# Kernel optimization log

Hardware: AMD Instinct MI355X
Metric: run time of the kernel (lower is better)

Reference implementation:

```python
import jax, jax.numpy as jnp
import numpy as np

NUM_HEADS = 12


def setup_inputs() -> dict:
    key = jax.random.key(0)
    k1, k2, k3, k4 = jax.random.split(key, 4)
    B, N, C = 8, 1024, 768
    x = jax.random.normal(k1, (B, N, C), dtype=jnp.float32)
    w_qkv = jax.random.normal(k2, (3 * C, C), dtype=jnp.float32) * 0.02
    w_proj = jax.random.normal(k3, (C, C), dtype=jnp.float32) * 0.02
    b_proj = jax.random.normal(k4, (C,), dtype=jnp.float32) * 0.02
    return {"x": x, "w_qkv": w_qkv, "w_proj": w_proj, "b_proj": b_proj}


def reference(x, w_qkv, w_proj, b_proj):
    B, N, C = x.shape
    H = NUM_HEADS
    D = C // H
    scale = D ** -0.5
    # qkv projection (HMQLinear with quant=False is a plain linear, bias=False)
    qkv = jnp.einsum('bnc,oc->bno', x, w_qkv)          # [B,N,3C]
    qkv = qkv.reshape(B, N, 3, H, D).transpose(2, 0, 3, 1, 4)  # [3,B,H,N,D]
    q, k, v = qkv[0], qkv[1], qkv[2]
    # HMQMulQK (passthrough matmul), scale applied after QK^T as in source
    attn = jnp.einsum('bhqd,bhkd->bhqk', q, k) * scale  # [B,H,N,N]
    attn = jax.nn.softmax(attn, axis=-1)                # HMQSoftmax
    out = jnp.einsum('bhqk,bhkd->bhqd', attn, v)        # HMQMulSV
    out = out.transpose(0, 2, 1, 3).reshape(B, N, C)
    # output projection (HMQLinear, default bias=True)
    return jnp.einsum('bnc,oc->bno', out, w_proj) + b_proj
```

## Files before the change

kernel.cpp:

```cpp
#include <hip/hip_runtime.h>
#include <hip/hip_bf16.h>
#include <stdint.h>

typedef __attribute__((ext_vector_type(8))) short short8;
typedef __attribute__((ext_vector_type(4))) float f32x4;
typedef __attribute__((ext_vector_type(16))) float f32x16;
typedef __attribute__((ext_vector_type(4))) unsigned short us4;

__device__ inline unsigned short f2bf(float f) {
    unsigned int u = __float_as_uint(f);
    u += 0x7FFFu + ((u >> 16) & 1u);
    return (unsigned short)(u >> 16);
}

__device__ inline unsigned int cvtpk(float lo, float hi) {
    unsigned int r;
    asm("v_cvt_pk_bf16_f32 %0, %1, %2" : "=v"(r) : "v"(lo), "v"(hi));
    return r;
}

__device__ inline void pl32swap(unsigned int& a, unsigned int& b) {
    asm volatile("v_permlane32_swap_b32 %0, %1" : "+v"(a), "+v"(b));
}

__global__ void cvt_f32_bf16(const float* __restrict__ in,
                             unsigned short* __restrict__ out, int n4) {
    int i = blockIdx.x * blockDim.x + threadIdx.x;
    if (i >= n4) return;
    float4 v = ((const float4*)in)[i];
    us4 o;
    o.x = f2bf(v.x); o.y = f2bf(v.y); o.z = f2bf(v.z); o.w = f2bf(v.w);
    ((us4*)out)[i] = o;
}

#define BM 128
#define BN 128
#define BKK 32

template<int MODE>
__global__ __launch_bounds__(256)
void gemm_bt(const unsigned short* __restrict__ A,
             const unsigned short* __restrict__ Bm,
             unsigned short* __restrict__ Qo, unsigned short* __restrict__ Ko,
             unsigned short* __restrict__ Vto,
             float* __restrict__ Co, const float* __restrict__ bias,
             int M, int N, int K)
{
    __shared__ __align__(16) unsigned short As[2][BM * BKK];
    __shared__ __align__(16) unsigned short Bs[2][BN * BKK];
    const int tid = threadIdx.x;
    const int wave = tid >> 6, lane = tid & 63;
    const int tr = blockIdx.x * BM;
    const int tc = blockIdx.y * BN;
    const int wm = wave >> 1, wn = wave & 1;

    f32x4 acc[4][4] = {};

    const int srow = lane >> 2;
    const int scol = (lane & 3) * 8;

    auto stage = [&](int it, int buf) {
#pragma unroll
        for (int i = 0; i < 2; ++i) {
            int rb = (wave * 2 + i) * 16;
            __builtin_amdgcn_global_load_lds(
                (const __attribute__((address_space(1))) void*)(A + (size_t)(tr + rb + srow) * K + it * BKK + scol),
                (__attribute__((address_space(3))) void*)(&As[buf][rb * BKK]),
                16, 0, 0);
            __builtin_amdgcn_global_load_lds(
                (const __attribute__((address_space(1))) void*)(Bm + (size_t)(tc + rb + srow) * K + it * BKK + scol),
                (__attribute__((address_space(3))) void*)(&Bs[buf][rb * BKK]),
                16, 0, 0);
        }
    };

    const int nIt = K / BKK;
    stage(0, 0);
    __syncthreads();

    for (int it = 0; it < nIt; ++it) {
        const int cur = it & 1;
        if (it + 1 < nIt) stage(it + 1, cur ^ 1);

        short8 af[4], bf[4];
#pragma unroll
        for (int mt = 0; mt < 4; ++mt)
            af[mt] = *(const short8*)&As[cur][(wm * 64 + mt * 16 + (lane & 15)) * BKK + (lane >> 4) * 8];
#pragma unroll
        for (int nt = 0; nt < 4; ++nt)
            bf[nt] = *(const short8*)&Bs[cur][(wn * 64 + nt * 16 + (lane & 15)) * BKK + (lane >> 4) * 8];
#pragma unroll
        for (int mt = 0; mt < 4; ++mt)
#pragma unroll
            for (int nt = 0; nt < 4; ++nt)
                acc[mt][nt] = __builtin_amdgcn_mfma_f32_16x16x32_bf16(af[mt], bf[nt], acc[mt][nt], 0, 0, 0);
        __syncthreads();
    }

    const float QSCALE = 0.18033688011112042f;
#pragma unroll
    for (int mt = 0; mt < 4; ++mt) {
#pragma unroll
        for (int nt = 0; nt < 4; ++nt) {
            int col = tc + wn * 64 + nt * 16 + (lane & 15);
            int row0 = tr + wm * 64 + mt * 16 + (lane >> 4) * 4;
            if constexpr (MODE == 0) {
                int s = (col >= 1536) ? 2 : (col >= 768 ? 1 : 0);
                int rem = col - s * 768;
                int h = rem >> 6, d = rem & 63;
                int b = row0 >> 10, n0 = row0 & 1023;
                int bh = b * 12 + h;
                if (s == 2) {
                    us4 pv;
#pragma unroll
                    for (int r = 0; r < 4; ++r) pv[r] = f2bf(acc[mt][nt][r]);
                    *(us4*)&Vto[((size_t)bh * 64 + d) * 1024 + n0] = pv;
                } else {
                    unsigned short* dst = (s == 0) ? Qo : Ko;
                    float sc = (s == 0) ? QSCALE : 1.0f;
#pragma unroll
                    for (int r = 0; r < 4; ++r)
                        dst[((size_t)bh * 1024 + n0 + r) * 64 + d] = f2bf(acc[mt][nt][r] * sc);
                }
            } else {
#pragma unroll
                for (int r = 0; r < 4; ++r)
                    Co[(size_t)(row0 + r) * N + col] = acc[mt][nt][r] + bias[col];
            }
        }
    }
}

__global__ __launch_bounds__(256)
void attn_kernel(const unsigned short* __restrict__ Q,
                 const unsigned short* __restrict__ Kg,
                 const unsigned short* __restrict__ Vt,
                 unsigned short* __restrict__ Og)
{
    __shared__ __align__(16) unsigned short KV[2][2][64 * 64];

    const int tid = threadIdx.x;
    const int wave = tid >> 6, lane = tid & 63;
    const int l31 = lane & 31, hi = lane >> 5;
    const int bh = blockIdx.y;
    const int b = bh / 12, h = bh % 12;
    const size_t baseK = (size_t)bh * 1024 * 64;
    const size_t baseV = (size_t)bh * 64 * 1024;
    const int q0 = blockIdx.x * 128 + wave * 32;

    short8 qf[4];
#pragma unroll
    for (int ds = 0; ds < 4; ++ds)
        qf[ds] = *(const short8*)&Q[baseK + (size_t)(q0 + l31) * 64 + ds * 16 + hi * 8];

    f32x16 ot0 = {}, ot1 = {};
    float l = 0.f;

    auto stage = [&](int kt, int buf) {
        const unsigned short* gK = Kg + baseK + (size_t)kt * 64 * 64;
        const unsigned short* gV = Vt + baseV + kt * 64;
#pragma unroll
        for (int i = 0; i < 2; ++i) {
            int c = wave * 128 + i * 64 + lane;
            int r = c >> 3, cc = c & 7;
            int sw = (cc ^ (r & 7)) * 8;
            __builtin_amdgcn_global_load_lds(
                (const __attribute__((address_space(1))) void*)(gK + r * 64 + sw),
                (__attribute__((address_space(3))) void*)(&KV[buf][0][(wave * 128 + i * 64) * 8]),
                16, 0, 0);
            __builtin_amdgcn_global_load_lds(
                (const __attribute__((address_space(1))) void*)(gV + (size_t)r * 1024 + sw),
                (__attribute__((address_space(3))) void*)(&KV[buf][1][(wave * 128 + i * 64) * 8]),
                16, 0, 0);
        }
    };

    auto rfrag = [&](const unsigned short* s, int row, int cc) -> short8 {
        return *(const short8*)&s[(row * 8 + (cc ^ (row & 7))) * 8];
    };

    stage(0, 0);
    __syncthreads();

    for (int kt = 0; kt < 16; ++kt) {
        const int cur = kt & 1;
        if (kt < 15) stage(kt + 1, cur ^ 1);

        f32x16 st0 = {}, st1 = {};
        __builtin_amdgcn_s_setprio(1);
#pragma unroll
        for (int ds = 0; ds < 4; ++ds) {
            short8 k0 = rfrag(KV[cur][0], l31, ds * 2 + hi);
            short8 k1 = rfrag(KV[cur][0], 32 + l31, ds * 2 + hi);
            st0 = __builtin_amdgcn_mfma_f32_32x32x16_bf16(k0, qf[ds], st0, 0, 0, 0);
            st1 = __builtin_amdgcn_mfma_f32_32x32x16_bf16(k1, qf[ds], st1, 0, 0, 0);
        }
        __builtin_amdgcn_s_setprio(0);

#pragma unroll
        for (int i = 0; i < 16; ++i) {
            st0[i] = exp2f(st0[i]);
            st1[i] = exp2f(st1[i]);
        }
        float su[8];
#pragma unroll
        for (int i = 0; i < 8; ++i)
            su[i] = (st0[2 * i] + st0[2 * i + 1]) + (st1[2 * i] + st1[2 * i + 1]);
#pragma unroll
        for (int s = 4; s > 0; s >>= 1)
#pragma unroll
            for (int i = 0; i < 4; ++i)
                if (i < s) su[i] += su[i + s];
        float ps = su[0];
        {
            unsigned int pu = __float_as_uint(ps), pv = pu;
            pl32swap(pu, pv);
            float other = __uint_as_float(hi ? pv : pu);
            l += ps + other;
        }

        short8 paf[4];
#pragma unroll
        for (int kb = 0; kb < 4; ++kb) {
            unsigned int a0, a1, b0, b1;
            if (kb < 2) {
                int t0 = 8 * kb;
                a0 = cvtpk(st0[t0 + 0], st0[t0 + 1]);
                a1 = cvtpk(st0[t0 + 2], st0[t0 + 3]);
                b0 = cvtpk(st0[t0 + 4], st0[t0 + 5]);
                b1 = cvtpk(st0[t0 + 6], st0[t0 + 7]);
            } else {
                int t0 = 8 * (kb - 2);
                a0 = cvtpk(st1[t0 + 0], st1[t0 + 1]);
                a1 = cvtpk(st1[t0 + 2], st1[t0 + 3]);
                b0 = cvtpk(st1[t0 + 4], st1[t0 + 5]);
                b1 = cvtpk(st1[t0 + 6], st1[t0 + 7]);
            }
            pl32swap(a0, b0);
            pl32swap(a1, b1);
            union { unsigned int u[4]; short8 s; } fr;
            fr.u[0] = a0; fr.u[1] = a1; fr.u[2] = b0; fr.u[3] = b1;
            paf[kb] = fr.s;
        }

        __builtin_amdgcn_s_setprio(1);
#pragma unroll
        for (int kb = 0; kb < 4; ++kb) {
            short8 v0 = rfrag(KV[cur][1], l31, kb * 2 + hi);
            short8 v1 = rfrag(KV[cur][1], 32 + l31, kb * 2 + hi);
            ot0 = __builtin_amdgcn_mfma_f32_32x32x16_bf16(v0, paf[kb], ot0, 0, 0, 0);
            ot1 = __builtin_amdgcn_mfma_f32_32x32x16_bf16(v1, paf[kb], ot1, 0, 0, 0);
        }
        __builtin_amdgcn_s_setprio(0);

        __syncthreads();
    }

    float inv = 1.f / l;
#pragma unroll
    for (int i = 0; i < 16; ++i) { ot0[i] *= inv; ot1[i] *= inv; }

    unsigned int* ow = (unsigned int*)(&KV[0][0][0]) + wave * 1152;
#pragma unroll
    for (int dt = 0; dt < 2; ++dt)
#pragma unroll
        for (int rp = 0; rp < 8; ++rp) {
            unsigned int w = (dt == 0) ? cvtpk(ot0[2 * rp], ot0[2 * rp + 1])
                                       : cvtpk(ot1[2 * rp], ot1[2 * rp + 1]);
            int wd = dt * 16 + 4 * (rp >> 1) + 2 * hi + (rp & 1);
            ow[l31 * 36 + wd] = w;
        }
#pragma unroll
    for (int i = 0; i < 4; ++i) {
        int c = i * 64 + lane;
        int qr = c >> 3, ch = c & 7;
        short8 vv = *(const short8*)((const unsigned short*)&ow[qr * 36 + ch * 4]);
        *(short8*)&Og[(size_t)(b * 1024 + q0 + qr) * 768 + h * 64 + ch * 8] = vv;
    }
}

extern "C" void kernel_launch(void* const* d_in, const int* in_sizes, int n_in,
                              void* d_out, int out_size, void* d_ws, size_t ws_size,
                              hipStream_t stream) {
    const float* x      = (const float*)d_in[0];
    const float* w_qkv  = (const float*)d_in[1];
    const float* w_proj = (const float*)d_in[2];
    const float* b_proj = (const float*)d_in[3];
    float* out = (float*)d_out;

    const int Bb = 8, Nn = 1024, C = 768;
    const int M = Bb * Nn;
    const size_t XB = (size_t)M * C;
    const size_t WQ = (size_t)3 * C * C;
    const size_t WP = (size_t)C * C;
    const size_t QE = (size_t)96 * 1024 * 64;

    unsigned short* xb  = (unsigned short*)d_ws;
    unsigned short* wqb = xb + XB;
    unsigned short* wpb = wqb + WQ;
    unsigned short* Qb  = wpb + WP;
    unsigned short* Kb  = Qb + QE;
    unsigned short* Vtb = Kb + QE;
    unsigned short* AO  = Vtb + QE;

    cvt_f32_bf16<<<(int)(XB / 4 + 255) / 256, 256, 0, stream>>>(x, xb, (int)(XB / 4));
    cvt_f32_bf16<<<(int)(WQ / 4 + 255) / 256, 256, 0, stream>>>(w_qkv, wqb, (int)(WQ / 4));
    cvt_f32_bf16<<<(int)(WP / 4 + 255) / 256, 256, 0, stream>>>(w_proj, wpb, (int)(WP / 4));

    gemm_bt<0><<<dim3(M / BM, (3 * C) / BN), 256, 0, stream>>>(
        xb, wqb, Qb, Kb, Vtb, nullptr, nullptr, M, 3 * C, C);

    attn_kernel<<<dim3(Nn / 128, Bb * 12), 256, 0, stream>>>(Qb, Kb, Vtb, AO);

    gemm_bt<1><<<dim3(M / BM, C / BN), 256, 0, stream>>>(
        AO, wpb, nullptr, nullptr, nullptr, out, b_proj, M, C, C);
}
```

Before: 136.8 us.

## Permute V layout to drop permlane swaps, interleave softmax with PV MFMAs, fuse conversions

The V^T store in the QKV GEMM now permutes token positions within 16-element groups. This lets the attention kernel feed exp'd score registers straight into the PV MFMA without the permlane32 swaps. The attention loop is split so exp and pack of the first score tile overlap with PV MFMAs, and the row-sum cross-half reduction moves out of the loop. It also uses the native exp2 builtin, sets launch bounds for 3 blocks per CU, and merges the three f32-to-bf16 conversion launches into one. The risk is correctness: the layout permutation must exactly match the MFMA fragment mapping.

```diff
diff --git a/kernel.cpp b/kernel.cpp
--- a/kernel.cpp
+++ b/kernel.cpp
@@ -23,14 +23,29 @@
     asm volatile("v_permlane32_swap_b32 %0, %1" : "+v"(a), "+v"(b));
 }
 
-__global__ void cvt_f32_bf16(const float* __restrict__ in,
-                             unsigned short* __restrict__ out, int n4) {
+__device__ inline float fexp2(float x) {
+#if __has_builtin(__builtin_amdgcn_exp2f)
+    return __builtin_amdgcn_exp2f(x);
+#else
+    return exp2f(x);
+#endif
+}
+
+__global__ void cvt_all(const float* __restrict__ x, const float* __restrict__ wq,
+                        const float* __restrict__ wp,
+                        unsigned short* __restrict__ xb,
+                        unsigned short* __restrict__ wqb,
+                        unsigned short* __restrict__ wpb) {
+    const int X4 = 1572864, Q4 = 442368;
     int i = blockIdx.x * blockDim.x + threadIdx.x;
-    if (i >= n4) return;
-    float4 v = ((const float4*)in)[i];
+    const float* src; unsigned short* dst; int j;
+    if (i < X4) { src = x; dst = xb; j = i; }
+    else if (i < X4 + Q4) { src = wq; dst = wqb; j = i - X4; }
+    else { src = wp; dst = wpb; j = i - X4 - Q4; }
+    float4 v = ((const float4*)src)[j];
     us4 o;
     o.x = f2bf(v.x); o.y = f2bf(v.y); o.z = f2bf(v.z); o.w = f2bf(v.w);
-    ((us4*)out)[i] = o;
+    ((us4*)dst)[j] = o;
 }
 
 #define BM 128
@@ -114,7 +129,9 @@
                     us4 pv;
 #pragma unroll
                     for (int r = 0; r < 4; ++r) pv[r] = f2bf(acc[mt][nt][r]);
-                    *(us4*)&Vto[((size_t)bh * 64 + d) * 1024 + n0] = pv;
+                    int qd = (n0 >> 2) & 3;
+                    int nst = n0 + ((qd == 1) ? 4 : (qd == 2) ? -4 : 0);
+                    *(us4*)&Vto[((size_t)bh * 64 + d) * 1024 + nst] = pv;
                 } else {
                     unsigned short* dst = (s == 0) ? Qo : Ko;
                     float sc = (s == 0) ? QSCALE : 1.0f;
@@ -131,7 +148,7 @@
     }
 }
 
-__global__ __launch_bounds__(256)
+__global__ __launch_bounds__(256, 3)
 void attn_kernel(const unsigned short* __restrict__ Q,
                  const unsigned short* __restrict__ Kg,
                  const unsigned short* __restrict__ Vt,
@@ -179,6 +196,14 @@
         return *(const short8*)&s[(row * 8 + (cc ^ (row & 7))) * 8];
     };
 
+    auto pack8 = [&](const f32x16& S, int r0) -> short8 {
+        union { unsigned int u[4]; short8 s; } fr;
+#pragma unroll
+        for (int w = 0; w < 4; ++w)
+            fr.u[w] = cvtpk(S[r0 + 2 * w], S[r0 + 2 * w + 1]);
+        return fr.s;
+    };
+
     stage(0, 0);
     __syncthreads();
 
@@ -197,11 +222,39 @@
         }
         __builtin_amdgcn_s_setprio(0);
 
-#pragma unroll
-        for (int i = 0; i < 16; ++i) {
-            st0[i] = exp2f(st0[i]);
-            st1[i] = exp2f(st1[i]);
-        }
+        short8 v00 = rfrag(KV[cur][1], l31, 0 + hi);
+        short8 v10 = rfrag(KV[cur][1], 32 + l31, 0 + hi);
+        short8 v01 = rfrag(KV[cur][1], l31, 2 + hi);
+        short8 v11 = rfrag(KV[cur][1], 32 + l31, 2 + hi);
+
+#pragma unroll
+        for (int i = 0; i < 16; ++i) st0[i] = fexp2(st0[i]);
+        short8 paf0 = pack8(st0, 0);
+        short8 paf1 = pack8(st0, 8);
+
+        __builtin_amdgcn_s_setprio(1);
+        ot0 = __builtin_amdgcn_mfma_f32_32x32x16_bf16(v00, paf0, ot0, 0, 0, 0);
+        ot1 = __builtin_amdgcn_mfma_f32_32x32x16_bf16(v10, paf0, ot1, 0, 0, 0);
+        ot0 = __builtin_amdgcn_mfma_f32_32x32x16_bf16(v01, paf1, ot0, 0, 0, 0);
+        ot1 = __builtin_amdgcn_mfma_f32_32x32x16_bf16(v11, paf1, ot1, 0, 0, 0);
+        __builtin_amdgcn_s_setprio(0);
+
+        short8 v02 = rfrag(KV[cur][1], l31, 4 + hi);
+        short8 v12 = rfrag(KV[cur][1], 32 + l31, 4 + hi);
+        short8 v03 = rfrag(KV[cur][1], l31, 6 + hi);
+        short8 v13 = rfrag(KV[cur][1], 32 + l31, 6 + hi);
+#pragma unroll
+        for (int i = 0; i < 16; ++i) st1[i] = fexp2(st1[i]);
+        short8 paf2 = pack8(st1, 0);
+        short8 paf3 = pack8(st1, 8);
+
+        __builtin_amdgcn_s_setprio(1);
+        ot0 = __builtin_amdgcn_mfma_f32_32x32x16_bf16(v02, paf2, ot0, 0, 0, 0);
+        ot1 = __builtin_amdgcn_mfma_f32_32x32x16_bf16(v12, paf2, ot1, 0, 0, 0);
+        ot0 = __builtin_amdgcn_mfma_f32_32x32x16_bf16(v03, paf3, ot0, 0, 0, 0);
+        ot1 = __builtin_amdgcn_mfma_f32_32x32x16_bf16(v13, paf3, ot1, 0, 0, 0);
+        __builtin_amdgcn_s_setprio(0);
+
         float su[8];
 #pragma unroll
         for (int i = 0; i < 8; ++i)
@@ -211,49 +264,15 @@
 #pragma unroll
             for (int i = 0; i < 4; ++i)
                 if (i < s) su[i] += su[i + s];
-        float ps = su[0];
-        {
-            unsigned int pu = __float_as_uint(ps), pv = pu;
-            pl32swap(pu, pv);
-            float other = __uint_as_float(hi ? pv : pu);
-            l += ps + other;
-        }
-
-        short8 paf[4];
-#pragma unroll
-        for (int kb = 0; kb < 4; ++kb) {
-            unsigned int a0, a1, b0, b1;
-            if (kb < 2) {
-                int t0 = 8 * kb;
-                a0 = cvtpk(st0[t0 + 0], st0[t0 + 1]);
-                a1 = cvtpk(st0[t0 + 2], st0[t0 + 3]);
-                b0 = cvtpk(st0[t0 + 4], st0[t0 + 5]);
-                b1 = cvtpk(st0[t0 + 6], st0[t0 + 7]);
-            } else {
-                int t0 = 8 * (kb - 2);
-                a0 = cvtpk(st1[t0 + 0], st1[t0 + 1]);
-                a1 = cvtpk(st1[t0 + 2], st1[t0 + 3]);
-                b0 = cvtpk(st1[t0 + 4], st1[t0 + 5]);
-                b1 = cvtpk(st1[t0 + 6], st1[t0 + 7]);
-            }
-            pl32swap(a0, b0);
-            pl32swap(a1, b1);
-            union { unsigned int u[4]; short8 s; } fr;
-            fr.u[0] = a0; fr.u[1] = a1; fr.u[2] = b0; fr.u[3] = b1;
-            paf[kb] = fr.s;
-        }
-
-        __builtin_amdgcn_s_setprio(1);
-#pragma unroll
-        for (int kb = 0; kb < 4; ++kb) {
-            short8 v0 = rfrag(KV[cur][1], l31, kb * 2 + hi);
-            short8 v1 = rfrag(KV[cur][1], 32 + l31, kb * 2 + hi);
-            ot0 = __builtin_amdgcn_mfma_f32_32x32x16_bf16(v0, paf[kb], ot0, 0, 0, 0);
-            ot1 = __builtin_amdgcn_mfma_f32_32x32x16_bf16(v1, paf[kb], ot1, 0, 0, 0);
-        }
-        __builtin_amdgcn_s_setprio(0);
+        l += su[0];
 
         __syncthreads();
+    }
+
+    {
+        unsigned int pu = __float_as_uint(l), pv = pu;
+        pl32swap(pu, pv);
+        l += __uint_as_float(hi ? pv : pu);
     }
 
     float inv = 1.f / l;
@@ -303,9 +322,7 @@
     unsigned short* Vtb = Kb + QE;
     unsigned short* AO  = Vtb + QE;
 
-    cvt_f32_bf16<<<(int)(XB / 4 + 255) / 256, 256, 0, stream>>>(x, xb, (int)(XB / 4));
-    cvt_f32_bf16<<<(int)(WQ / 4 + 255) / 256, 256, 0, stream>>>(w_qkv, wqb, (int)(WQ / 4));
-    cvt_f32_bf16<<<(int)(WP / 4 + 255) / 256, 256, 0, stream>>>(w_proj, wpb, (int)(WP / 4));
+    cvt_all<<<8448, 256, 0, stream>>>(x, w_qkv, w_proj, xb, wqb, wpb);
 
     gemm_bt<0><<<dim3(M / BM, (3 * C) / BN), 256, 0, stream>>>(
         xb, wqb, Qb, Kb, Vtb, nullptr, nullptr, M, 3 * C, C);
```

Result: faster. 116.3 us (-15.0%).
